# Performance work log

Measured on AMD Instinct MI355X. Metric: run time of the kernel, lower is better.

Reference implementation:

```python
import jax, jax.numpy as jnp
import numpy as np

EXTENT = 3.0            # 'radius' arg of the model is passed as extents to ContinuousConv
SEARCH_R = EXTENT / 2.0 # Open3D fixed_radius_search uses extents/2
KS = 6                  # kernel_size [6,6,6]
N, K = 10000, 32
EPS = 1e-12
FOUR_OVER_PI = float(4.0 / np.pi)


def ball_to_cube_volume_preserving(u):
    # u: [...,3] in the unit ball -> cube [-1,1]^3 (Open3D mapping:
    # MapSphereToCylinder followed by MapCylinderToCube).
    x, y, z = u[..., 0], u[..., 1], u[..., 2]
    sq = x * x + y * y + z * z
    norm = jnp.sqrt(jnp.maximum(sq, EPS))
    rho2 = x * x + y * y
    # sphere -> cylinder (volume preserving, two regions)
    in_cone = 1.25 * z * z > rho2
    s1 = jnp.sqrt(3.0 * norm / (norm + jnp.abs(z)))
    s2 = norm / jnp.sqrt(jnp.maximum(rho2, EPS))
    s = jnp.where(in_cone, s1, s2)
    xc = x * s
    yc = y * s
    zc = jnp.where(in_cone, jnp.sign(z) * norm, 1.5 * z)
    tiny = sq < EPS
    xc = jnp.where(tiny, 0.0, xc)
    yc = jnp.where(tiny, 0.0, yc)
    zc = jnp.where(tiny, 0.0, zc)
    # cylinder -> cube (inverse concentric / Shirley-Chiu map on xy disc)
    sq_xy = xc * xc + yc * yc
    norm_xy = jnp.sqrt(jnp.maximum(sq_xy, EPS))
    x_major = jnp.abs(yc) <= jnp.abs(xc)
    xd = jnp.where(jnp.abs(xc) < EPS, 1.0, xc)
    yd = jnp.where(jnp.abs(yc) < EPS, 1.0, yc)
    tx = jnp.sign(xc) * norm_xy
    ty = jnp.sign(yc) * norm_xy
    xq = jnp.where(x_major, tx, ty * FOUR_OVER_PI * jnp.arctan(xc / yd))
    yq = jnp.where(x_major, tx * FOUR_OVER_PI * jnp.arctan(yc / xd), ty)
    tiny_xy = sq_xy < EPS
    xq = jnp.where(tiny_xy, 0.0, xq)
    yq = jnp.where(tiny_xy, 0.0, yq)
    return jnp.stack([xq, yq, zc], axis=-1)


def continuous_conv(feats, pos, nidx, nmask, W, b):
    # feats [N,Cin], pos [N,3], nidx [N,K] int32 (padded), nmask [N,K] bool
    # W [KS,KS,KS,Cin,Cout], b [Cout]
    n, k = nidx.shape
    Cin, Cout = W.shape[3], W.shape[4]
    M = KS * KS * KS
    maskf = nmask.astype(feats.dtype)
    u = (pos[nidx] - pos[:, None, :]) * (2.0 / EXTENT)          # [N,K,3], unit ball
    coords = (ball_to_cube_volume_preserving(u) + 1.0) * (0.5 * (KS - 1))  # align_corners
    i0f = jnp.floor(coords)
    frac = coords - i0f
    i0 = jnp.clip(i0f.astype(jnp.int32), 0, KS - 1)
    i1 = jnp.minimum(i0 + 1, KS - 1)
    fN = feats[nidx]                                            # [N,K,Cin]
    base = jnp.arange(n, dtype=jnp.int32)[:, None] * M          # [N,1]
    # Scatter trilinear-weighted neighbor features into per-point kernel cells:
    # A[j, cell, :] = sum_{neighbors k, corners c} w_{j,k,c} * feats[nidx[j,k]]
    A = jnp.zeros((n * M, Cin), feats.dtype)
    for cx in (0, 1):
        ix = i1[..., 0] if cx else i0[..., 0]
        wx = frac[..., 0] if cx else 1.0 - frac[..., 0]
        for cy in (0, 1):
            iy = i1[..., 1] if cy else i0[..., 1]
            wy = frac[..., 1] if cy else 1.0 - frac[..., 1]
            for cz in (0, 1):
                iz = i1[..., 2] if cz else i0[..., 2]
                wz = frac[..., 2] if cz else 1.0 - frac[..., 2]
                w = wx * wy * wz * maskf                        # [N,K]
                flat = (base + (ix * KS + iy) * KS + iz).reshape(-1)
                A = A.at[flat].add((w[..., None] * fN).reshape(n * k, Cin))
    out = jnp.einsum('nmc,mco->no', A.reshape(n, M, Cin), W.reshape(M, Cin, Cout))
    # normalize=True (Open3D default): divide by neighbor count, guarded for empty
    cnt = maskf.sum(axis=1, keepdims=True)
    out = jnp.where(cnt > 0, out / jnp.maximum(cnt, 1.0), out)
    return jax.nn.relu(out + b)                                 # use_bias + activation


def setup_inputs() -> dict:
    rng = np.random.default_rng(0)
    L = 16.0  # box side -> ~32 neighbors on average within SEARCH_R
    pos = (rng.random((N, 3)) * L).astype(np.float32)
    nidx = np.zeros((N, K), np.int32)
    nmask = np.zeros((N, K), bool)
    chunk = 512
    for s in range(0, N, chunk):
        d2 = ((pos[s:s + chunk, None, :] - pos[None, :, :]) ** 2).sum(-1)
        part = np.argpartition(d2, K, axis=1)[:, :K].astype(np.int32)
        m = np.take_along_axis(d2, part, axis=1) <= SEARCH_R * SEARCH_R
        nidx[s:s + chunk] = np.where(m, part, 0)
        nmask[s:s + chunk] = m

    def p(*shape):
        return jnp.asarray((rng.standard_normal(shape) * 0.1).astype(np.float32))

    return {
        'feats': jnp.asarray(rng.standard_normal((N, 4)).astype(np.float32)),
        'pos': jnp.asarray(pos),
        'neighbor_idx': jnp.asarray(nidx),
        'neighbor_mask': jnp.asarray(nmask),
        'W1': p(KS, KS, KS, 4, 64), 'b1': jnp.zeros((64,), jnp.float32),
        'W2': p(KS, KS, KS, 64, 64), 'b2': jnp.zeros((64,), jnp.float32),
        'W3': p(KS, KS, KS, 64, 32), 'b3': jnp.zeros((32,), jnp.float32),
        'Wfc1': p(32, 64), 'bfc1': jnp.zeros((64,), jnp.float32),
        'Wfc2': p(64, 64), 'bfc2': jnp.zeros((64,), jnp.float32),
        'Wfc3': p(64, 32), 'bfc3': jnp.zeros((32,), jnp.float32),
        'Wout': p(32, 3), 'bout': jnp.zeros((3,), jnp.float32),
    }


def reference(feats, pos, neighbor_idx, neighbor_mask, W1, b1, W2, b2, W3, b3,
              Wfc1, bfc1, Wfc2, bfc2, Wfc3, bfc3, Wout, bout):
    x = continuous_conv(feats, pos, neighbor_idx, neighbor_mask, W1, b1)
    x = continuous_conv(x, pos, neighbor_idx, neighbor_mask, W2, b2)
    x = continuous_conv(x, pos, neighbor_idx, neighbor_mask, W3, b3)
    x = jax.nn.relu(x @ Wfc1 + bfc1)
    x = jax.nn.relu(x @ Wfc2 + bfc2)
    x = jax.nn.relu(x @ Wfc3 + bfc3)
    return x @ Wout + bout
```

## Files before the change

### kernel.cpp

```cpp
#include <hip/hip_runtime.h>
#include <math.h>

#define NPTS  10000
#define KNB   32
#define NCELL 216
#define NSGT  157

__device__ __forceinline__ float sgnf(float v) {
    return (v > 0.0f) ? 1.0f : ((v < 0.0f) ? -1.0f : 0.0f);
}

__device__ __forceinline__ void ball_to_cube(float x, float y, float z,
                                             float& X, float& Y, float& Z) {
    const float EPSF = 1e-12f;
    const float FOPI = (float)(4.0 / 3.14159265358979323846);
    float sq   = x * x + y * y + z * z;
    float norm = sqrtf(fmaxf(sq, EPSF));
    float rho2 = x * x + y * y;
    bool in_cone = (1.25f * z * z > rho2);
    float s1 = sqrtf(3.0f * norm / (norm + fabsf(z)));
    float s2 = norm / sqrtf(fmaxf(rho2, EPSF));
    float s  = in_cone ? s1 : s2;
    float xc = x * s;
    float yc = y * s;
    float zc = in_cone ? sgnf(z) * norm : 1.5f * z;
    if (sq < EPSF) { xc = 0.0f; yc = 0.0f; zc = 0.0f; }
    float sq_xy   = xc * xc + yc * yc;
    float norm_xy = sqrtf(fmaxf(sq_xy, EPSF));
    bool x_major = (fabsf(yc) <= fabsf(xc));
    float xd = (fabsf(xc) < EPSF) ? 1.0f : xc;
    float yd = (fabsf(yc) < EPSF) ? 1.0f : yc;
    float tx = sgnf(xc) * norm_xy;
    float ty = sgnf(yc) * norm_xy;
    float xq = x_major ? tx : ty * FOPI * atanf(xc / yd);
    float yq = x_major ? tx * FOPI * atanf(yc / xd) : ty;
    if (sq_xy < EPSF) { xq = 0.0f; yq = 0.0f; }
    X = xq; Y = yq; Z = zc;
}

__global__ __launch_bounds__(256) void geom_kernel(
    const float* __restrict__ pos, const int* __restrict__ nidx,
    uint4* __restrict__ geo, float* __restrict__ cnt) {
    int t = blockIdx.x * 256 + threadIdx.x;
    if (t >= NPTS * KNB) return;
    int j = t >> 5;
    int k = t & 31;
    int nid = nidx[t];
    float px = pos[j * 3], py = pos[j * 3 + 1], pz = pos[j * 3 + 2];
    float qx = pos[nid * 3], qy = pos[nid * 3 + 1], qz = pos[nid * 3 + 2];
    float dx = __fsub_rn(px, qx), dy = __fsub_rn(py, qy), dz = __fsub_rn(pz, qz);
    float d2 = __fadd_rn(__fadd_rn(__fmul_rn(dx, dx), __fmul_rn(dy, dy)),
                         __fmul_rn(dz, dz));
    bool valid = (d2 <= 2.25f);
    if (valid && nid == 0) {
        for (int kk = 0; kk < k; ++kk) {
            if (nidx[j * KNB + kk] == 0) { valid = false; break; }
        }
    }
    uint4 g = make_uint4(0u, 0u, 0u, 0u);
    if (valid) {
        const float C = (float)(2.0 / 3.0);
        float ux = (qx - px) * C, uy = (qy - py) * C, uz = (qz - pz) * C;
        float X, Y, Z;
        ball_to_cube(ux, uy, uz, X, Y, Z);
        float cs[3] = { (X + 1.0f) * 2.5f, (Y + 1.0f) * 2.5f, (Z + 1.0f) * 2.5f };
        int i0[3], i1[3];
        float fr[3];
        #pragma unroll
        for (int d = 0; d < 3; ++d) {
            float f0 = floorf(cs[d]);
            fr[d] = cs[d] - f0;
            int a = (int)f0;
            a = min(max(a, 0), 5);
            i0[d] = a;
            i1[d] = min(a + 1, 5);
        }
        int c000 = (i0[0] * 6 + i0[1]) * 6 + i0[2];
        unsigned bits = (unsigned)c000
                      | ((unsigned)(i1[0] - i0[0]) << 8)
                      | ((unsigned)(i1[1] - i0[1]) << 9)
                      | ((unsigned)(i1[2] - i0[2]) << 10)
                      | (1u << 11)
                      | ((unsigned)nid << 12);
        g.x = __float_as_uint(fr[0]);
        g.y = __float_as_uint(fr[1]);
        g.z = __float_as_uint(fr[2]);
        g.w = bits;
        atomicAdd(&cnt[j], 1.0f);
    }
    geo[t] = g;
}

__global__ __launch_bounds__(256) void sort_kernel(
    const uint4* __restrict__ geo, uint2* __restrict__ contribs,
    int* __restrict__ starts) {
    __shared__ int hist[NCELL];
    __shared__ int pref[NCELL + 1];
    const int sg = blockIdx.x, tid = threadIdx.x;
    if (tid < NCELL) hist[tid] = 0;
    __syncthreads();
    const int npts = min(64, NPTS - sg * 64);
    const int nrec = npts * KNB;
    const uint4* gb = geo + (size_t)sg * 64 * KNB;
    for (int r = tid; r < nrec; r += 256) {
        uint4 g = gb[r];
        if (g.w & 2048u) {
            int c000 = g.w & 255u;
            int dxo = (g.w & 256u)  ? 36 : 0;
            int dyo = (g.w & 512u)  ? 6  : 0;
            int dzo = (g.w & 1024u) ? 1  : 0;
            #pragma unroll
            for (int c = 0; c < 8; ++c) {
                int cell = c000 + ((c & 4) ? dxo : 0) + ((c & 2) ? dyo : 0)
                                + ((c & 1) ? dzo : 0);
                atomicAdd(&hist[cell], 1);
            }
        }
    }
    __syncthreads();
    if (tid == 0) {
        int run = 0;
        for (int m = 0; m < NCELL; ++m) { pref[m] = run; run += hist[m]; }
        pref[NCELL] = run;
    }
    __syncthreads();
    for (int i = tid; i < NCELL + 1; i += 256)
        starts[sg * (NCELL + 1) + i] = pref[i];
    if (tid < NCELL) hist[tid] = pref[tid];
    __syncthreads();
    uint2* cb = contribs + (size_t)sg * 16384;
    for (int r = tid; r < nrec; r += 256) {
        uint4 g = gb[r];
        if (g.w & 2048u) {
            int ptl = r >> 5;
            float fx = __uint_as_float(g.x);
            float fy = __uint_as_float(g.y);
            float fz = __uint_as_float(g.z);
            int c000 = g.w & 255u;
            int dxo = (g.w & 256u)  ? 36 : 0;
            int dyo = (g.w & 512u)  ? 6  : 0;
            int dzo = (g.w & 1024u) ? 1  : 0;
            int nid = (g.w >> 12) & 16383u;
            #pragma unroll
            for (int c = 0; c < 8; ++c) {
                float wgt = ((c & 4) ? fx : 1.f - fx)
                          * ((c & 2) ? fy : 1.f - fy)
                          * ((c & 1) ? fz : 1.f - fz);
                int cell = c000 + ((c & 4) ? dxo : 0) + ((c & 2) ? dyo : 0)
                                + ((c & 1) ? dzo : 0);
                int p = atomicAdd(&hist[cell], 1);
                cb[p] = make_uint2(__float_as_uint(wgt),
                                   (unsigned)nid | ((unsigned)ptl << 14)
                                                 | ((unsigned)cell << 20));
            }
        }
    }
}

template<int CIN, int COUT, int CPC, int MT, int KSPLIT>
__global__ __launch_bounds__(256, 3) void conv_kernel(
    const float* __restrict__ feats, const float* __restrict__ W,
    const uint2* __restrict__ contribs, const int* __restrict__ starts,
    float* __restrict__ partial) {
    constexpr int KC   = CPC * CIN;
    constexpr int ASTR = KC + 4;
    constexpr int CG   = COUT / 4;
    constexpr int NSG  = MT / 64;
    constexpr int NCHUNK = NCELL / CPC;
    constexpr int WPT  = (KC * COUT) / 1024;
    constexpr int TPC  = CIN / 4;
    constexpr int GPB  = 256 / TPC;

    __shared__ alignas(16) float Al[MT * ASTR];
    __shared__ alignas(16) float Wl[2][KC * COUT];
    __shared__ int Sl[NSG][NCELL + 1];

    const int tid   = threadIdx.x;
    const int cg    = tid % CG;
    const int pg    = tid / CG;
    const int bx    = blockIdx.x;
    const int ks    = blockIdx.y;
    const int gslot = tid / TPC;
    const int ch    = tid % TPC;

    for (int s2 = 0; s2 < NSG; ++s2) {
        int sg = bx * NSG + s2;
        for (int i = tid; i < NCELL + 1; i += 256)
            Sl[s2][i] = (sg < NSGT) ? starts[sg * (NCELL + 1) + i] : 0;
    }

    const int c0 = NCHUNK * ks / KSPLIT;
    const int c1 = NCHUNK * (ks + 1) / KSPLIT;

    auto stage = [&](int c) {
        float4 z4; z4.x = z4.y = z4.z = z4.w = 0.f;
        float4* Az = reinterpret_cast<float4*>(Al);
        #pragma unroll 4
        for (int i = tid; i < MT * (ASTR / 4); i += 256) Az[i] = z4;
        __syncthreads();
        const int cellbase = c * CPC;
        #pragma unroll
        for (int s2 = 0; s2 < NSG; ++s2) {
            const uint2* cbs = contribs + (size_t)(bx * NSG + s2) * 16384;
            const int s = Sl[s2][cellbase];
            const int e = Sl[s2][cellbase + CPC];
            for (int i = s + gslot; i < e; i += GPB) {
                uint2 rec = cbs[i];
                float wgt = __uint_as_float(rec.x);
                int nid = rec.y & 16383;
                int ptl = (rec.y >> 14) & 63;
                int cel = (rec.y >> 20);
                float4 f4 = *reinterpret_cast<const float4*>(
                    feats + (size_t)nid * CIN + ch * 4);
                float* dst = Al + (s2 * 64 + ptl) * ASTR
                           + (cel - cellbase) * CIN + ch * 4;
                atomicAdd(dst + 0, wgt * f4.x);
                atomicAdd(dst + 1, wgt * f4.y);
                atomicAdd(dst + 2, wgt * f4.z);
                atomicAdd(dst + 3, wgt * f4.w);
            }
        }
    };

    {
        const float4* Wg = reinterpret_cast<const float4*>(W + (size_t)c0 * KC * COUT);
        float4* Wd = reinterpret_cast<float4*>(Wl[0]);
        #pragma unroll
        for (int j = 0; j < WPT; ++j) Wd[tid + j * 256] = Wg[tid + j * 256];
    }
    stage(c0);
    __syncthreads();

    float4 acc[4];
    #pragma unroll
    for (int p = 0; p < 4; ++p) { acc[p].x = acc[p].y = acc[p].z = acc[p].w = 0.f; }

    for (int c = c0; c < c1; ++c) {
        const int b = (c - c0) & 1;
        float4 wpre[WPT];
        if (c + 1 < c1) {
            const float4* Wg = reinterpret_cast<const float4*>(W + (size_t)(c + 1) * KC * COUT);
            #pragma unroll
            for (int j = 0; j < WPT; ++j) wpre[j] = Wg[tid + j * 256];
        }
        const float* Wb = Wl[b];
        #pragma unroll 2
        for (int g = 0; g < KC / 4; ++g) {
            float4 wf[4];
            #pragma unroll
            for (int j = 0; j < 4; ++j)
                wf[j] = *reinterpret_cast<const float4*>(Wb + (g * 4 + j) * COUT + cg * 4);
            float4 af[4];
            #pragma unroll
            for (int p = 0; p < 4; ++p)
                af[p] = *reinterpret_cast<const float4*>(Al + (pg * 4 + p) * ASTR + g * 4);
            #pragma unroll
            for (int p = 0; p < 4; ++p) {
                const float* afp = reinterpret_cast<const float*>(&af[p]);
                #pragma unroll
                for (int j = 0; j < 4; ++j) {
                    float a = afp[j];
                    acc[p].x = fmaf(a, wf[j].x, acc[p].x);
                    acc[p].y = fmaf(a, wf[j].y, acc[p].y);
                    acc[p].z = fmaf(a, wf[j].z, acc[p].z);
                    acc[p].w = fmaf(a, wf[j].w, acc[p].w);
                }
            }
        }
        __syncthreads();
        if (c + 1 < c1) {
            float4* Wd = reinterpret_cast<float4*>(Wl[b ^ 1]);
            #pragma unroll
            for (int j = 0; j < WPT; ++j) Wd[tid + j * 256] = wpre[j];
            stage(c + 1);
        }
        __syncthreads();
    }

    #pragma unroll
    for (int p = 0; p < 4; ++p) {
        int n = bx * MT + pg * 4 + p;
        if (n < NPTS)
            *reinterpret_cast<float4*>(partial + ((size_t)ks * NPTS + n) * COUT + cg * 4) = acc[p];
    }
}

template<int COUT, int KSPLIT>
__global__ __launch_bounds__(256) void combine_kernel(
    const float* __restrict__ partial, const float* __restrict__ cnt,
    const float* __restrict__ bias, float* __restrict__ out) {
    int idx = blockIdx.x * 256 + threadIdx.x;
    if (idx >= NPTS * COUT) return;
    int n = idx / COUT, co = idx % COUT;
    float s = 0.f;
    #pragma unroll
    for (int k2 = 0; k2 < KSPLIT; ++k2)
        s += partial[((size_t)k2 * NPTS + n) * COUT + co];
    float c = cnt[n];
    if (c > 0.f) s /= fmaxf(c, 1.f);
    out[idx] = fmaxf(s + bias[co], 0.f);
}

__global__ __launch_bounds__(64) void fc_kernel(
    const float* __restrict__ x,
    const float* __restrict__ W1, const float* __restrict__ b1,
    const float* __restrict__ W2, const float* __restrict__ b2,
    const float* __restrict__ W3, const float* __restrict__ b3,
    const float* __restrict__ W4, const float* __restrict__ b4,
    float* __restrict__ out) {
    int n = blockIdx.x;
    int lane = threadIdx.x;
    float xv = (lane < 32) ? x[(size_t)n * 32 + lane] : 0.0f;

    float t = b1[lane];
    for (int ci = 0; ci < 32; ++ci)
        t = fmaf(__shfl(xv, ci), W1[ci * 64 + lane], t);
    float h1 = fmaxf(t, 0.0f);

    t = b2[lane];
    for (int ci = 0; ci < 64; ++ci)
        t = fmaf(__shfl(h1, ci), W2[ci * 64 + lane], t);
    float h2 = fmaxf(t, 0.0f);

    int l32 = lane & 31;
    t = b3[l32];
    for (int ci = 0; ci < 64; ++ci)
        t = fmaf(__shfl(h2, ci), W3[ci * 32 + l32], t);
    float h3 = fmaxf(t, 0.0f);

    int ch = (lane < 3) ? lane : 0;
    float o = b4[ch];
    for (int ci = 0; ci < 32; ++ci)
        o = fmaf(__shfl(h3, ci), W4[ci * 3 + ch], o);
    if (lane < 3) out[(size_t)n * 3 + lane] = o;
}

extern "C" void kernel_launch(void* const* d_in, const int* in_sizes, int n_in,
                              void* d_out, int out_size, void* d_ws, size_t ws_size,
                              hipStream_t stream) {
    const float* feats = (const float*)d_in[0];
    const float* pos   = (const float*)d_in[1];
    const int*   nidx  = (const int*)d_in[2];
    const float* W1 = (const float*)d_in[4];
    const float* b1 = (const float*)d_in[5];
    const float* W2 = (const float*)d_in[6];
    const float* b2 = (const float*)d_in[7];
    const float* W3 = (const float*)d_in[8];
    const float* b3 = (const float*)d_in[9];
    const float* Wfc1 = (const float*)d_in[10];
    const float* bfc1 = (const float*)d_in[11];
    const float* Wfc2 = (const float*)d_in[12];
    const float* bfc2 = (const float*)d_in[13];
    const float* Wfc3 = (const float*)d_in[14];
    const float* bfc3 = (const float*)d_in[15];
    const float* Wout = (const float*)d_in[16];
    const float* bout = (const float*)d_in[17];

    char* ws = (char*)d_ws;
    uint2* contrib = (uint2*)(ws);
    int*   starts  = (int*)  (ws + 20578304);
    float* cnt     = (float*)(ws + 20714624);
    float* x1      = (float*)(ws + 20754624);
    float* x2      = (float*)(ws + 23314624);
    float* x3      = (float*)(ws + 25874624);
    uint4* geo     = (uint4*)(ws + 27154624);
    float* partial = (float*)(ws + 27154624);

    hipMemsetAsync(cnt, 0, NPTS * sizeof(float), stream);
    geom_kernel<<<(NPTS * KNB) / 256, 256, 0, stream>>>(pos, nidx, geo, cnt);
    sort_kernel<<<NSGT, 256, 0, stream>>>(geo, contrib, starts);

    conv_kernel<4, 64, 8, 64, 2><<<dim3(157, 2), 256, 0, stream>>>(
        feats, W1, contrib, starts, partial);
    combine_kernel<64, 2><<<(NPTS * 64 + 255) / 256, 256, 0, stream>>>(
        partial, cnt, b1, x1);

    conv_kernel<64, 64, 1, 64, 4><<<dim3(157, 4), 256, 0, stream>>>(
        x1, W2, contrib, starts, partial);
    combine_kernel<64, 4><<<(NPTS * 64 + 255) / 256, 256, 0, stream>>>(
        partial, cnt, b2, x2);

    conv_kernel<64, 32, 1, 128, 4><<<dim3(79, 4), 256, 0, stream>>>(
        x2, W3, contrib, starts, partial);
    combine_kernel<32, 4><<<(NPTS * 32 + 255) / 256, 256, 0, stream>>>(
        partial, cnt, b3, x3);

    fc_kernel<<<NPTS, 64, 0, stream>>>(x3, Wfc1, bfc1, Wfc2, bfc2,
                                       Wfc3, bfc3, Wout, bout, (float*)d_out);
}
```

Before: 2.580 ms.

## Restructure continuous conv: per-wave output columns, global weights, double-buffered scatter

The conv kernel now uses COUT*8 threads per block, with each wave owning 8 output channels and each lane one point. Weights are read directly from global memory with wave-uniform addresses instead of being staged in LDS. The A tile is double-buffered, so the scatter for the next chunk runs before the current chunk's matmul, removing a barrier and the LDS weight copy. K-split factors are raised to 4/8 for more parallelism, with a workspace-size check choosing between configurations for layer 2. The costs are more partial-sum traffic and more global weight reads per block.

```diff
diff --git a/kernel.cpp b/kernel.cpp
--- a/kernel.cpp
+++ b/kernel.cpp
@@ -157,131 +157,105 @@
     }
 }
 
-template<int CIN, int COUT, int CPC, int MT, int KSPLIT>
-__global__ __launch_bounds__(256, 3) void conv_kernel(
+template<int CIN, int COUT, int CPC, int KSPLIT>
+__global__ __launch_bounds__(COUT * 8, 6) void conv_kernel(
     const float* __restrict__ feats, const float* __restrict__ W,
     const uint2* __restrict__ contribs, const int* __restrict__ starts,
     float* __restrict__ partial) {
     constexpr int KC   = CPC * CIN;
     constexpr int ASTR = KC + 4;
-    constexpr int CG   = COUT / 4;
-    constexpr int NSG  = MT / 64;
+    constexpr int BT   = COUT * 8;
     constexpr int NCHUNK = NCELL / CPC;
-    constexpr int WPT  = (KC * COUT) / 1024;
     constexpr int TPC  = CIN / 4;
-    constexpr int GPB  = 256 / TPC;
-
-    __shared__ alignas(16) float Al[MT * ASTR];
-    __shared__ alignas(16) float Wl[2][KC * COUT];
-    __shared__ int Sl[NSG][NCELL + 1];
+    constexpr int GPB  = BT / TPC;
+
+    __shared__ alignas(16) float Ab[2][64 * ASTR];
 
     const int tid   = threadIdx.x;
-    const int cg    = tid % CG;
-    const int pg    = tid / CG;
+    const int lane  = tid & 63;
+    const int wvid  = __builtin_amdgcn_readfirstlane(tid >> 6);
+    const int cow   = wvid * 8;
     const int bx    = blockIdx.x;
     const int ks    = blockIdx.y;
     const int gslot = tid / TPC;
     const int ch    = tid % TPC;
 
-    for (int s2 = 0; s2 < NSG; ++s2) {
-        int sg = bx * NSG + s2;
-        for (int i = tid; i < NCELL + 1; i += 256)
-            Sl[s2][i] = (sg < NSGT) ? starts[sg * (NCELL + 1) + i] : 0;
-    }
+    const uint2* cbs = contribs + (size_t)bx * 16384;
+    const int*   st  = starts + bx * (NCELL + 1);
 
     const int c0 = NCHUNK * ks / KSPLIT;
     const int c1 = NCHUNK * (ks + 1) / KSPLIT;
 
-    auto stage = [&](int c) {
-        float4 z4; z4.x = z4.y = z4.z = z4.w = 0.f;
-        float4* Az = reinterpret_cast<float4*>(Al);
-        #pragma unroll 4
-        for (int i = tid; i < MT * (ASTR / 4); i += 256) Az[i] = z4;
-        __syncthreads();
-        const int cellbase = c * CPC;
-        #pragma unroll
-        for (int s2 = 0; s2 < NSG; ++s2) {
-            const uint2* cbs = contribs + (size_t)(bx * NSG + s2) * 16384;
-            const int s = Sl[s2][cellbase];
-            const int e = Sl[s2][cellbase + CPC];
-            for (int i = s + gslot; i < e; i += GPB) {
-                uint2 rec = cbs[i];
-                float wgt = __uint_as_float(rec.x);
-                int nid = rec.y & 16383;
-                int ptl = (rec.y >> 14) & 63;
-                int cel = (rec.y >> 20);
-                float4 f4 = *reinterpret_cast<const float4*>(
-                    feats + (size_t)nid * CIN + ch * 4);
-                float* dst = Al + (s2 * 64 + ptl) * ASTR
-                           + (cel - cellbase) * CIN + ch * 4;
-                atomicAdd(dst + 0, wgt * f4.x);
-                atomicAdd(dst + 1, wgt * f4.y);
-                atomicAdd(dst + 2, wgt * f4.z);
-                atomicAdd(dst + 3, wgt * f4.w);
-            }
-        }
+    auto zero = [&](int b) {
+        float4 z; z.x = z.y = z.z = z.w = 0.f;
+        float4* p = reinterpret_cast<float4*>(Ab[b]);
+        #pragma unroll 2
+        for (int i = tid; i < 64 * ASTR / 4; i += BT) p[i] = z;
     };
-
-    {
-        const float4* Wg = reinterpret_cast<const float4*>(W + (size_t)c0 * KC * COUT);
-        float4* Wd = reinterpret_cast<float4*>(Wl[0]);
-        #pragma unroll
-        for (int j = 0; j < WPT; ++j) Wd[tid + j * 256] = Wg[tid + j * 256];
-    }
-    stage(c0);
-    __syncthreads();
-
-    float4 acc[4];
+    auto scatter = [&](int c, int b) {
+        const int s = st[c * CPC], e = st[c * CPC + CPC];
+        const int cb4 = c * CPC;
+        for (int i = s + gslot; i < e; i += GPB) {
+            uint2 rec = cbs[i];
+            float wgt = __uint_as_float(rec.x);
+            int nid = rec.y & 16383;
+            int ptl = (rec.y >> 14) & 63;
+            int cel = (int)(rec.y >> 20);
+            float4 f4 = *reinterpret_cast<const float4*>(
+                feats + (size_t)nid * CIN + ch * 4);
+            float* dst = &Ab[b][ptl * ASTR + (cel - cb4) * CIN + ch * 4];
+            atomicAdd(dst + 0, wgt * f4.x);
+            atomicAdd(dst + 1, wgt * f4.y);
+            atomicAdd(dst + 2, wgt * f4.z);
+            atomicAdd(dst + 3, wgt * f4.w);
+        }
+    };
+
+    zero(0); zero(1);
+    __syncthreads();
+    scatter(c0, 0);
+    __syncthreads();
+
+    float acc[8];
     #pragma unroll
-    for (int p = 0; p < 4; ++p) { acc[p].x = acc[p].y = acc[p].z = acc[p].w = 0.f; }
+    for (int j = 0; j < 8; ++j) acc[j] = 0.f;
 
     for (int c = c0; c < c1; ++c) {
         const int b = (c - c0) & 1;
-        float4 wpre[WPT];
-        if (c + 1 < c1) {
-            const float4* Wg = reinterpret_cast<const float4*>(W + (size_t)(c + 1) * KC * COUT);
+        if (c + 1 < c1) scatter(c + 1, b ^ 1);
+        const float* Wc = W + (size_t)c * CPC * CIN * COUT;
+        const float* Ar = Ab[b] + lane * ASTR;
+        #pragma unroll 4
+        for (int g = 0; g < KC / 4; ++g) {
+            float4 a4 = *reinterpret_cast<const float4*>(Ar + g * 4);
+            const float av[4] = { a4.x, a4.y, a4.z, a4.w };
             #pragma unroll
-            for (int j = 0; j < WPT; ++j) wpre[j] = Wg[tid + j * 256];
-        }
-        const float* Wb = Wl[b];
-        #pragma unroll 2
-        for (int g = 0; g < KC / 4; ++g) {
-            float4 wf[4];
-            #pragma unroll
-            for (int j = 0; j < 4; ++j)
-                wf[j] = *reinterpret_cast<const float4*>(Wb + (g * 4 + j) * COUT + cg * 4);
-            float4 af[4];
-            #pragma unroll
-            for (int p = 0; p < 4; ++p)
-                af[p] = *reinterpret_cast<const float4*>(Al + (pg * 4 + p) * ASTR + g * 4);
-            #pragma unroll
-            for (int p = 0; p < 4; ++p) {
-                const float* afp = reinterpret_cast<const float*>(&af[p]);
-                #pragma unroll
-                for (int j = 0; j < 4; ++j) {
-                    float a = afp[j];
-                    acc[p].x = fmaf(a, wf[j].x, acc[p].x);
-                    acc[p].y = fmaf(a, wf[j].y, acc[p].y);
-                    acc[p].z = fmaf(a, wf[j].z, acc[p].z);
-                    acc[p].w = fmaf(a, wf[j].w, acc[p].w);
-                }
+            for (int j = 0; j < 4; ++j) {
+                float4 w0 = *reinterpret_cast<const float4*>(
+                    Wc + (size_t)(g * 4 + j) * COUT + cow);
+                float4 w1 = *reinterpret_cast<const float4*>(
+                    Wc + (size_t)(g * 4 + j) * COUT + cow + 4);
+                float a = av[j];
+                acc[0] = fmaf(a, w0.x, acc[0]);
+                acc[1] = fmaf(a, w0.y, acc[1]);
+                acc[2] = fmaf(a, w0.z, acc[2]);
+                acc[3] = fmaf(a, w0.w, acc[3]);
+                acc[4] = fmaf(a, w1.x, acc[4]);
+                acc[5] = fmaf(a, w1.y, acc[5]);
+                acc[6] = fmaf(a, w1.z, acc[6]);
+                acc[7] = fmaf(a, w1.w, acc[7]);
             }
         }
         __syncthreads();
-        if (c + 1 < c1) {
-            float4* Wd = reinterpret_cast<float4*>(Wl[b ^ 1]);
-            #pragma unroll
-            for (int j = 0; j < WPT; ++j) Wd[tid + j * 256] = wpre[j];
-            stage(c + 1);
-        }
+        zero(b);
         __syncthreads();
     }
 
-    #pragma unroll
-    for (int p = 0; p < 4; ++p) {
-        int n = bx * MT + pg * 4 + p;
-        if (n < NPTS)
-            *reinterpret_cast<float4*>(partial + ((size_t)ks * NPTS + n) * COUT + cg * 4) = acc[p];
+    const int n = bx * 64 + lane;
+    if (n < NPTS) {
+        float* po = partial + ((size_t)ks * NPTS + n) * COUT + cow;
+        *reinterpret_cast<float4*>(po)     = make_float4(acc[0], acc[1], acc[2], acc[3]);
+        *reinterpret_cast<float4*>(po + 4) = make_float4(acc[4], acc[5], acc[6], acc[7]);
     }
 }
 
@@ -366,23 +340,32 @@
     uint4* geo     = (uint4*)(ws + 27154624);
     float* partial = (float*)(ws + 27154624);
 
+    const bool big = ws_size >= (size_t)47634624;
+
     hipMemsetAsync(cnt, 0, NPTS * sizeof(float), stream);
     geom_kernel<<<(NPTS * KNB) / 256, 256, 0, stream>>>(pos, nidx, geo, cnt);
     sort_kernel<<<NSGT, 256, 0, stream>>>(geo, contrib, starts);
 
-    conv_kernel<4, 64, 8, 64, 2><<<dim3(157, 2), 256, 0, stream>>>(
+    conv_kernel<4, 64, 8, 4><<<dim3(NSGT, 4), 512, 0, stream>>>(
         feats, W1, contrib, starts, partial);
-    combine_kernel<64, 2><<<(NPTS * 64 + 255) / 256, 256, 0, stream>>>(
+    combine_kernel<64, 4><<<(NPTS * 64 + 255) / 256, 256, 0, stream>>>(
         partial, cnt, b1, x1);
 
-    conv_kernel<64, 64, 1, 64, 4><<<dim3(157, 4), 256, 0, stream>>>(
-        x1, W2, contrib, starts, partial);
-    combine_kernel<64, 4><<<(NPTS * 64 + 255) / 256, 256, 0, stream>>>(
-        partial, cnt, b2, x2);
-
-    conv_kernel<64, 32, 1, 128, 4><<<dim3(79, 4), 256, 0, stream>>>(
+    if (big) {
+        conv_kernel<64, 64, 1, 8><<<dim3(NSGT, 8), 512, 0, stream>>>(
+            x1, W2, contrib, starts, partial);
+        combine_kernel<64, 8><<<(NPTS * 64 + 255) / 256, 256, 0, stream>>>(
+            partial, cnt, b2, x2);
+    } else {
+        conv_kernel<64, 64, 1, 4><<<dim3(NSGT, 4), 512, 0, stream>>>(
+            x1, W2, contrib, starts, partial);
+        combine_kernel<64, 4><<<(NPTS * 64 + 255) / 256, 256, 0, stream>>>(
+            partial, cnt, b2, x2);
+    }
+
+    conv_kernel<64, 32, 1, 8><<<dim3(NSGT, 8), 256, 0, stream>>>(
         x2, W3, contrib, starts, partial);
-    combine_kernel<32, 4><<<(NPTS * 32 + 255) / 256, 256, 0, stream>>>(
+    combine_kernel<32, 8><<<(NPTS * 32 + 255) / 256, 256, 0, stream>>>(
         partial, cnt, b3, x3);
 
     fc_kernel<<<NPTS, 64, 0, stream>>>(x3, Wfc1, bfc1, Wfc2, bfc2,
```

New measurement: 2.078 ms. -19.5%, faster.
